# Performance work log

Hardware: AMD Instinct MI355X
Metric: run time of the kernel (lower is better)

The kernel has to match this reference:

```python
import jax, jax.numpy as jnp
import numpy as np

B, N, C, H = 2, 2048, 1024, 16
D = C // H
NEG = -1e9  # keras Softmax large negative for masked positions


def setup_inputs() -> dict:
    key = jax.random.key(0)
    ks = jax.random.split(key, 10)
    s = lambda fan_in: 1.0 / np.sqrt(fan_in)
    return {
        "x": jax.random.normal(ks[0], (B, N, C), jnp.float32),
        "mask": jnp.ones((B, 1, 1, N), jnp.bool_),
        "Wqkv": jax.random.normal(ks[1], (C, 3 * C), jnp.float32) * s(C),
        "bqkv": jnp.zeros((3 * C,), jnp.float32),
        "Wl": jax.random.normal(ks[2], (H, H), jnp.float32) * s(H),
        "bl": jnp.zeros((H,), jnp.float32),
        "Ww": jax.random.normal(ks[3], (H, H), jnp.float32) * s(H),
        "bw": jnp.zeros((H,), jnp.float32),
        "Wp": jax.random.normal(ks[4], (C, C), jnp.float32) * s(C),
        "bp": jnp.zeros((C,), jnp.float32),
    }


def reference(x, mask, Wqkv, bqkv, Wl, bl, Ww, bw, Wp, bp):
    scale = jnp.asarray(D ** -0.5, x.dtype)
    qkv = x @ Wqkv + bqkv                                  # [B,N,3C]
    qkv = qkv.reshape(B, N, 3, H, D).transpose(2, 0, 3, 1, 4)  # [3,B,H,N,D]
    q, k, v = qkv[0] * scale, qkv[1], qkv[2]
    attn = jnp.einsum("bhnd,bhmd->bhnm", q, k)             # [B,H,N,N]
    # pre-softmax talking-heads: mix head axis
    attn = jnp.einsum("bhnm,hg->bgnm", attn, Wl) + bl[None, :, None, None]
    # keras Softmax with boolean mask: add -1e9 where mask is False
    attn = attn + (1.0 - mask.astype(attn.dtype)) * NEG
    attn = jax.nn.softmax(attn, axis=-1)
    # post-softmax talking-heads
    attn = jnp.einsum("bhnm,hg->bgnm", attn, Ww) + bw[None, :, None, None]
    out = jnp.einsum("bhnm,bhmd->bhnd", attn, v)           # [B,H,N,D]
    out = out.transpose(0, 2, 1, 3).reshape(B, N, C)
    return out @ Wp + bp
```

## Files before the change

kernel.cpp:

```cpp
#include <hip/hip_runtime.h>
#include <hip/hip_bf16.h>


typedef __bf16 bf16_t;
typedef __bf16 bf16x8 __attribute__((ext_vector_type(8)));
typedef float f32x4 __attribute__((ext_vector_type(4)));

#define DEV static __device__ __forceinline__

static constexpr float NEGV = -1e9f;

DEV f32x4 mfma16(bf16x8 a, bf16x8 b, f32x4 c) {
  return __builtin_amdgcn_mfma_f32_16x16x32_bf16(a, b, c, 0, 0, 0);
}

DEV bf16x8 zero8() {
  bf16x8 z;
#pragma unroll
  for (int j = 0; j < 8; ++j) z[j] = (bf16_t)0.0f;
  return z;
}

DEV uint32_t pkbf(float lo, float hi) {
  union { bf16_t f; unsigned short s; } a, b;
  a.f = (bf16_t)lo; b.f = (bf16_t)hi;
  return (uint32_t)a.s | ((uint32_t)b.s << 16);
}

union U84 { uint32_t u[4]; bf16x8 v; };

__global__ __launch_bounds__(256) void mask_prep(const unsigned char* __restrict__ raw,
                                                 unsigned char* __restrict__ canon,
                                                 unsigned char* __restrict__ allflag) {
  __shared__ int c0, c12, f0, f1;
  const int tid = threadIdx.x;
  if (tid == 0) { c0 = 0; c12 = 0; f0 = 1; f1 = 1; }
  __syncthreads();
  int l0 = 0, l12 = 0;
  for (int i = tid; i < 4096; i += 256) {
    unsigned char v = raw[i];
    if (v) {
      int r = i & 3;
      if (r == 0) l0++;
      else if (r < 3) l12++;
    }
  }
  if (l0) atomicAdd(&c0, l0);
  if (l12) atomicAdd(&c12, l12);
  __syncthreads();
  const int mode = (c0 == 0) ? 2 : ((c12 > 0) ? 0 : 1);
  for (int i = tid; i < 4096; i += 256) {
    bool t;
    if (mode == 0)      t = raw[i] != 0;
    else if (mode == 1) t = ((const int*)raw)[i] != 0;
    else                t = ((const float*)raw)[i] != 0.0f;
    canon[i] = t ? 1 : 0;
    if (!t) atomicAnd(i < 2048 ? &f0 : &f1, 0);
  }
  __syncthreads();
  if (tid == 0) { allflag[0] = (unsigned char)f0; allflag[1] = (unsigned char)f1; }
}

__global__ __launch_bounds__(256) void gemm_kernel(
    const float* __restrict__ Af, const bf16_t* __restrict__ Ab,
    const float* __restrict__ Bw, const float* __restrict__ bias,
    float* __restrict__ outf,
    bf16_t* __restrict__ Qs, bf16_t* __restrict__ Ks, bf16_t* __restrict__ Vt,
    int K, int Nn, int epi) {
  __shared__ bf16_t As[64][40];
  __shared__ bf16_t Bs[64][40];
  const int tid = threadIdx.x;
  const int lane = tid & 63, wid = tid >> 6;
  const int bx = blockIdx.x, by = blockIdx.y;
  const int wr = (wid >> 1) * 32, wc = (wid & 1) * 32;
  const int lr = lane & 15, kq = lane >> 4;

  f32x4 acc[2][2];
#pragma unroll
  for (int i = 0; i < 2; ++i)
#pragma unroll
    for (int j = 0; j < 2; ++j) acc[i][j] = (f32x4){0.f, 0.f, 0.f, 0.f};

  for (int kt = 0; kt < K; kt += 32) {
    {
      const int row = tid >> 2, c8 = (tid & 3) * 8;
      if (epi == 0) {
        const float* p = Af + (size_t)(bx * 64 + row) * K + kt + c8;
        float4 v0 = *(const float4*)p;
        float4 v1 = *(const float4*)(p + 4);
        bf16x8 v;
        v[0] = (bf16_t)v0.x; v[1] = (bf16_t)v0.y; v[2] = (bf16_t)v0.z; v[3] = (bf16_t)v0.w;
        v[4] = (bf16_t)v1.x; v[5] = (bf16_t)v1.y; v[6] = (bf16_t)v1.z; v[7] = (bf16_t)v1.w;
        *(bf16x8*)&As[row][c8] = v;
      } else {
        *(bf16x8*)&As[row][c8] =
            *(const bf16x8*)(Ab + (size_t)(bx * 64 + row) * K + kt + c8);
      }
      const int krow = tid >> 3, n8 = (tid & 7) * 8;
      const float* bp = Bw + (size_t)(kt + krow) * Nn + by * 64 + n8;
      float4 b0 = *(const float4*)bp;
      float4 b1 = *(const float4*)(bp + 4);
      Bs[n8 + 0][krow] = (bf16_t)b0.x; Bs[n8 + 1][krow] = (bf16_t)b0.y;
      Bs[n8 + 2][krow] = (bf16_t)b0.z; Bs[n8 + 3][krow] = (bf16_t)b0.w;
      Bs[n8 + 4][krow] = (bf16_t)b1.x; Bs[n8 + 5][krow] = (bf16_t)b1.y;
      Bs[n8 + 6][krow] = (bf16_t)b1.z; Bs[n8 + 7][krow] = (bf16_t)b1.w;
    }
    __syncthreads();
#pragma unroll
    for (int rt = 0; rt < 2; ++rt) {
      bf16x8 af = *(const bf16x8*)&As[wr + rt * 16 + lr][kq * 8];
#pragma unroll
      for (int ct = 0; ct < 2; ++ct) {
        bf16x8 bf = *(const bf16x8*)&Bs[wc + ct * 16 + lr][kq * 8];
        acc[rt][ct] = mfma16(af, bf, acc[rt][ct]);
      }
    }
    __syncthreads();
  }

#pragma unroll
  for (int rt = 0; rt < 2; ++rt)
#pragma unroll
    for (int ct = 0; ct < 2; ++ct)
#pragma unroll
      for (int r = 0; r < 4; ++r) {
        const int grow = bx * 64 + wr + rt * 16 + kq * 4 + r;
        const int gcol = by * 64 + wc + ct * 16 + lr;
        const float v = acc[rt][ct][r] + bias[gcol];
        if (epi == 0) {
          const int t = gcol >> 10, h = (gcol >> 6) & 15, d = gcol & 63;
          const int b = grow >> 11, n = grow & 2047;
          if (t == 0)
            Qs[(((size_t)b * 16 + h) * 2048 + n) * 64 + d] = (bf16_t)(v * 0.125f);
          else if (t == 1)
            Ks[(((size_t)b * 16 + h) * 2048 + n) * 64 + d] = (bf16_t)v;
          else
            Vt[(((size_t)b * 16 + h) * 64 + d) * 2048 + n] = (bf16_t)v;
        } else {
          outf[(size_t)grow * Nn + gcol] = v;
        }
      }
}

__global__ __launch_bounds__(256) void vsum_kernel(const bf16_t* __restrict__ Vt,
                                                   float* __restrict__ Vsum) {
  const int lane = threadIdx.x & 63, wid = threadIdx.x >> 6;
  const int row = blockIdx.x * 4 + wid;
  const bf16_t* p = Vt + (size_t)row * 2048;
  float s = 0.f;
#pragma unroll
  for (int it = 0; it < 4; ++it) {
    bf16x8 v = *(const bf16x8*)(p + it * 512 + lane * 8);
#pragma unroll
    for (int j = 0; j < 8; ++j) s += (float)v[j];
  }
#pragma unroll
  for (int off = 32; off; off >>= 1) s += __shfl_xor(s, off);
  if (lane == 0) Vsum[row] = s;
}

__global__ __launch_bounds__(256, 2) void attn_pass1(
    const bf16_t* __restrict__ Qs, const bf16_t* __restrict__ Ks,
    const unsigned char* __restrict__ canon, const unsigned char* __restrict__ allflag,
    const float* __restrict__ Wl, const float* __restrict__ bl,
    float* __restrict__ pstats) {
  __shared__ uint32_t Sb[2][5120];
  const int tid = threadIdx.x, lane = tid & 63, wid = tid >> 6;
  const int c = lane & 15, kq = lane >> 4;
  const int job = (blockIdx.x & 7) * 128 + (blockIdx.x >> 3);
  const int mc = job >> 8, b = (job >> 7) & 1, nt = job & 127;
  const int n0 = nt * 16, mbeg = mc * 512;
  const int h0 = 4 * wid;
  const bool allt = allflag[b] != 0;

  bf16x8 wlf;
#pragma unroll
  for (int j = 0; j < 8; ++j) {
    const int k = kq * 8 + j;
    wlf[j] = (k < 16) ? (bf16_t)Wl[k * 16 + c] : (bf16_t)0.0f;
  }
  f32x4 blv;
#pragma unroll
  for (int r = 0; r < 4; ++r) blv[r] = bl[kq * 4 + r];

  bf16x8 qf[4][2];
#pragma unroll
  for (int hh = 0; hh < 4; ++hh)
#pragma unroll
    for (int ks = 0; ks < 2; ++ks)
      qf[hh][ks] = *(const bf16x8*)(Qs + ((size_t)(b * 16 + h0 + hh) * 2048 + n0 + c) *
                                             64 + ks * 32 + kq * 8);

  auto stage = [&](int v, uint32_t* sb) {
    const int m0 = mbeg + v * 32;
#pragma unroll
    for (int hp = 0; hp < 2; ++hp) {
      bf16x8 kf[2][2][2];
#pragma unroll
      for (int h2 = 0; h2 < 2; ++h2)
#pragma unroll
        for (int mt = 0; mt < 2; ++mt)
#pragma unroll
          for (int ks = 0; ks < 2; ++ks)
            kf[h2][mt][ks] =
                *(const bf16x8*)(Ks + ((size_t)(b * 16 + h0 + hp * 2 + h2) * 2048 +
                                       m0 + mt * 16 + c) * 64 + ks * 32 + kq * 8);
#pragma unroll
      for (int mt = 0; mt < 2; ++mt) {
        f32x4 a0 = (f32x4){0.f, 0.f, 0.f, 0.f};
        f32x4 a1 = (f32x4){0.f, 0.f, 0.f, 0.f};
        a0 = mfma16(qf[hp * 2 + 0][0], kf[0][mt][0], a0);
        a0 = mfma16(qf[hp * 2 + 0][1], kf[0][mt][1], a0);
        a1 = mfma16(qf[hp * 2 + 1][0], kf[1][mt][0], a1);
        a1 = mfma16(qf[hp * 2 + 1][1], kf[1][mt][1], a1);
#pragma unroll
        for (int r = 0; r < 4; ++r) {
          const int p = (kq * 4 + r) * 32 + mt * 16 + c;
          sb[p * 10 + ((2 * wid + hp) ^ (kq & 1))] = pkbf(a0[r], a1[r]);
        }
      }
    }
  };

  auto gatherS = [&](const uint32_t* sb, int pp) {
    const int prow = (wid * 8 + pp) * 16 + c;
    const int bp = (prow >> 7) & 1;
    if (kq < 2) {
      U84 t;
#pragma unroll
      for (int i = 0; i < 4; ++i) t.u[i] = sb[prow * 10 + ((kq * 4 + i) ^ bp)];
      return t.v;
    }
    return zero8();
  };

  float lacc[4][4];
#pragma unroll
  for (int r = 0; r < 4; ++r)
#pragma unroll
    for (int ns = 0; ns < 4; ++ns) lacc[r][ns] = 0.f;

  stage(0, Sb[0]);
  __syncthreads();
  for (int u = 0; u < 16; ++u) {
#pragma unroll
    for (int pp = 0; pp < 8; ++pp) {
      bf16x8 sf = gatherS(Sb[u & 1], pp);
      f32x4 d1 = mfma16(wlf, sf, blv);
      if (!allt && !canon[b * 2048 + mbeg + u * 32 + (pp & 1) * 16 + c]) {
        d1[0] += NEGV; d1[1] += NEGV; d1[2] += NEGV; d1[3] += NEGV;
      }
      const int ns = pp >> 1;
#pragma unroll
      for (int r = 0; r < 4; ++r) lacc[r][ns] += __expf(d1[r]);
    }
    if (u < 15) stage(u + 1, Sb[(u + 1) & 1]);
    __syncthreads();
  }

#pragma unroll
  for (int r = 0; r < 4; ++r)
#pragma unroll
    for (int ns = 0; ns < 4; ++ns) {
      float s = lacc[r][ns];
      s += __shfl_xor(s, 1);
      s += __shfl_xor(s, 2);
      s += __shfl_xor(s, 4);
      s += __shfl_xor(s, 8);
      if (c == 0)
        pstats[((size_t)(b * 4 + mc) * 2048 + n0 + wid * 4 + ns) * 16 + kq * 4 + r] = s;
    }
}

__global__ __launch_bounds__(256) void stats_merge(const float* __restrict__ ps,
                                                   float* __restrict__ fin) {
  const int i = blockIdx.x * 256 + threadIdx.x;
  const int b = i >> 15, rest = i & 32767;
  float s = 0.f;
#pragma unroll
  for (int ch = 0; ch < 4; ++ch) s += ps[((size_t)(b * 4 + ch) << 15) + rest];
  fin[i] = 1.0f / s;
}

__global__ __launch_bounds__(256, 2) void attn_pass2(
    const bf16_t* __restrict__ Qs, const bf16_t* __restrict__ Ks,
    const bf16_t* __restrict__ Vt, const unsigned char* __restrict__ canon,
    const unsigned char* __restrict__ allflag,
    const float* __restrict__ Wl, const float* __restrict__ bl,
    const float* __restrict__ Ww, const float* __restrict__ fin,
    float* __restrict__ Opart) {
  __shared__ uint32_t Sb[2][5120];
  __shared__ uint32_t Fb[2][16 * 260];
  const int tid = threadIdx.x, lane = tid & 63, wid = tid >> 6;
  const int c = lane & 15, kq = lane >> 4;
  const int job = (blockIdx.x & 7) * 64 + (blockIdx.x >> 3);
  const int mc = job >> 8, b = (job >> 7) & 1, nt = job & 127;
  const int n0 = nt * 16, mbeg = mc * 1024;
  const int h0 = 4 * wid;
  const bool allt = allflag[b] != 0;

  bf16x8 wlf, wwf;
#pragma unroll
  for (int j = 0; j < 8; ++j) {
    const int k = kq * 8 + j;
    wlf[j] = (k < 16) ? (bf16_t)Wl[k * 16 + c] : (bf16_t)0.0f;
    wwf[j] = (k < 16) ? (bf16_t)Ww[k * 16 + c] : (bf16_t)0.0f;
  }
  f32x4 blv;
#pragma unroll
  for (int r = 0; r < 4; ++r) blv[r] = bl[kq * 4 + r];

  float4 ivv[4];
#pragma unroll
  for (int ns = 0; ns < 4; ++ns)
    ivv[ns] =
        *(const float4*)&fin[((size_t)b * 2048 + n0 + wid * 4 + ns) * 16 + kq * 4];

  bf16x8 qf[4][2];
#pragma unroll
  for (int hh = 0; hh < 4; ++hh)
#pragma unroll
    for (int ks = 0; ks < 2; ++ks)
      qf[hh][ks] = *(const bf16x8*)(Qs + ((size_t)(b * 16 + h0 + hh) * 2048 + n0 + c) *
                                             64 + ks * 32 + kq * 8);

  auto stage = [&](int v, uint32_t* sb) {
    const int m0 = mbeg + v * 32;
#pragma unroll
    for (int hp = 0; hp < 2; ++hp) {
      bf16x8 kf[2][2][2];
#pragma unroll
      for (int h2 = 0; h2 < 2; ++h2)
#pragma unroll
        for (int mt = 0; mt < 2; ++mt)
#pragma unroll
          for (int ks = 0; ks < 2; ++ks)
            kf[h2][mt][ks] =
                *(const bf16x8*)(Ks + ((size_t)(b * 16 + h0 + hp * 2 + h2) * 2048 +
                                       m0 + mt * 16 + c) * 64 + ks * 32 + kq * 8);
#pragma unroll
      for (int mt = 0; mt < 2; ++mt) {
        f32x4 a0 = (f32x4){0.f, 0.f, 0.f, 0.f};
        f32x4 a1 = (f32x4){0.f, 0.f, 0.f, 0.f};
        a0 = mfma16(qf[hp * 2 + 0][0], kf[0][mt][0], a0);
        a0 = mfma16(qf[hp * 2 + 0][1], kf[0][mt][1], a0);
        a1 = mfma16(qf[hp * 2 + 1][0], kf[1][mt][0], a1);
        a1 = mfma16(qf[hp * 2 + 1][1], kf[1][mt][1], a1);
#pragma unroll
        for (int r = 0; r < 4; ++r) {
          const int p = (kq * 4 + r) * 32 + mt * 16 + c;
          sb[p * 10 + ((2 * wid + hp) ^ (kq & 1))] = pkbf(a0[r], a1[r]);
        }
      }
    }
  };

  auto gatherS = [&](const uint32_t* sb, int pp) {
    const int prow = (wid * 8 + pp) * 16 + c;
    const int bp = (prow >> 7) & 1;
    if (kq < 2) {
      U84 t;
#pragma unroll
      for (int i = 0; i < 4; ++i) t.u[i] = sb[prow * 10 + ((kq * 4 + i) ^ bp)];
      return t.v;
    }
    return zero8();
  };

  f32x4 oacc[4][4];
#pragma unroll
  for (int i = 0; i < 4; ++i)
#pragma unroll
    for (int j = 0; j < 4; ++j) oacc[i][j] = (f32x4){0.f, 0.f, 0.f, 0.f};

  stage(0, Sb[0]);
  __syncthreads();
  for (int u = 0; u < 32; ++u) {
    const uint32_t* scur = Sb[u & 1];
    uint32_t* snxt = Sb[(u + 1) & 1];
    bf16_t* fcur = (bf16_t*)Fb[u & 1];
    const uint32_t* fprev = Fb[(u + 1) & 1];
    if (u > 0) {
#pragma unroll
      for (int hh = 0; hh < 4; ++hh) {
        const int g2 = h0 + hh;
        bf16x8 af = *(const bf16x8*)&fprev[g2 * 260 + c * 16 + ((kq ^ (c & 3)) << 2)];
#pragma unroll
        for (int dt = 0; dt < 4; ++dt) {
          bf16x8 vf = *(const bf16x8*)(Vt + ((size_t)(b * 16 + g2) * 64 + dt * 16 + c) *
                                                2048 + mbeg + (u - 1) * 32 + kq * 8);
          oacc[hh][dt] = mfma16(af, vf, oacc[hh][dt]);
        }
      }
    }
#pragma unroll
    for (int pp = 0; pp < 8; ++pp) {
      bf16x8 sf = gatherS(scur, pp);
      f32x4 d1 = mfma16(wlf, sf, blv);
      if (!allt && !canon[b * 2048 + mbeg + u * 32 + (pp & 1) * 16 + c]) {
        d1[0] += NEGV; d1[1] += NEGV; d1[2] += NEGV; d1[3] += NEGV;
      }
      const int ns = pp >> 1;
      const float e0 = __expf(d1[0]) * ivv[ns].x;
      const float e1 = __expf(d1[1]) * ivv[ns].y;
      const float e2 = __expf(d1[2]) * ivv[ns].z;
      const float e3 = __expf(d1[3]) * ivv[ns].w;
      const uint32_t Aw = pkbf(e0, e1);
      const uint32_t Bw2 = pkbf(e2, e3);
      const int s0 = (c + 32 * kq) & 63;
      const int s1 = (s0 + 16) & 63;
      U84 ef;
      ef.u[0] = (uint32_t)__shfl((int)Aw, s0);
      ef.u[1] = (uint32_t)__shfl((int)Bw2, s0);
      ef.u[2] = (uint32_t)__shfl((int)Aw, s1);
      ef.u[3] = (uint32_t)__shfl((int)Bw2, s1);
      bf16x8 efv = (kq < 2) ? ef.v : zero8();
      f32x4 d2 = mfma16(wwf, efv, (f32x4){0.f, 0.f, 0.f, 0.f});
      const int pg = wid * 8 + pp;
      const int nl = pg >> 1, ml = (pg & 1) * 16 + c;
      const int wm = (ml >> 1) ^ ((nl & 3) << 2);
#pragma unroll
      for (int r = 0; r < 4; ++r)
        fcur[(kq * 4 + r) * 520 + nl * 32 + wm * 2 + (ml & 1)] = (bf16_t)d2[r];
    }
    if (u < 31) stage(u + 1, snxt);
    __syncthreads();
  }
  {
    const uint32_t* fprev = Fb[1];
#pragma unroll
    for (int hh = 0; hh < 4; ++hh) {
      const int g2 = h0 + hh;
      bf16x8 af = *(const bf16x8*)&fprev[g2 * 260 + c * 16 + ((kq ^ (c & 3)) << 2)];
#pragma unroll
      for (int dt = 0; dt < 4; ++dt) {
        bf16x8 vf = *(const bf16x8*)(Vt + ((size_t)(b * 16 + g2) * 64 + dt * 16 + c) *
                                              2048 + mbeg + 31 * 32 + kq * 8);
        oacc[hh][dt] = mfma16(af, vf, oacc[hh][dt]);
      }
    }
  }

#pragma unroll
  for (int hh = 0; hh < 4; ++hh)
#pragma unroll
    for (int dt = 0; dt < 4; ++dt)
#pragma unroll
      for (int r = 0; r < 4; ++r) {
        const int n = n0 + kq * 4 + r;
        const int col = (h0 + hh) * 64 + dt * 16 + c;
        Opart[(((size_t)b * 2 + mc) * 2048 + n) * 1024 + col] = oacc[hh][dt][r];
      }
}

__global__ __launch_bounds__(256) void reduce_ao(const float* __restrict__ Opart,
                                                 const float* __restrict__ bw,
                                                 const float* __restrict__ Vsum,
                                                 bf16_t* __restrict__ AO) {
  const size_t i = ((size_t)blockIdx.x * 256 + threadIdx.x) * 4;
  const int c = (int)(i & 1023), n = (int)((i >> 10) & 2047), b = (int)(i >> 21);
  const float4 p0 = *(const float4*)&Opart[(((size_t)b * 2 + 0) * 2048 + n) * 1024 + c];
  const float4 p1 = *(const float4*)&Opart[(((size_t)b * 2 + 1) * 2048 + n) * 1024 + c];
  float vv[4] = {p0.x + p1.x, p0.y + p1.y, p0.z + p1.z, p0.w + p1.w};
#pragma unroll
  for (int j = 0; j < 4; ++j) {
    const int cj = c + j, g2 = cj >> 6, d = cj & 63;
    AO[i + j] = (bf16_t)(vv[j] + bw[g2] * Vsum[((size_t)b * 16 + g2) * 64 + d]);
  }
}

extern "C" void kernel_launch(void* const* d_in, const int* in_sizes, int n_in,
                              void* d_out, int out_size, void* d_ws, size_t ws_size,
                              hipStream_t stream) {
  const float* x = (const float*)d_in[0];
  const unsigned char* mask = (const unsigned char*)d_in[1];
  const float* Wqkv = (const float*)d_in[2];
  const float* bqkv = (const float*)d_in[3];
  const float* Wl = (const float*)d_in[4];
  const float* bl = (const float*)d_in[5];
  const float* Ww = (const float*)d_in[6];
  const float* bw = (const float*)d_in[7];
  const float* Wp = (const float*)d_in[8];
  const float* bp = (const float*)d_in[9];
  float* out = (float*)d_out;

  char* w = (char*)d_ws;
  auto alloc = [&](size_t bytes) {
    char* p = w;
    w += (bytes + 255) & ~(size_t)255;
    return p;
  };
  bf16_t* Qs = (bf16_t*)alloc((size_t)2 * 16 * 2048 * 64 * 2);
  bf16_t* Ks = (bf16_t*)alloc((size_t)2 * 16 * 2048 * 64 * 2);
  bf16_t* Vt = (bf16_t*)alloc((size_t)2 * 16 * 2048 * 64 * 2);
  bf16_t* AO = (bf16_t*)alloc((size_t)4096 * 1024 * 2);
  float* Opart = (float*)alloc((size_t)4 * 2048 * 1024 * 4);
  float* pstats = (float*)alloc((size_t)8 * 2048 * 16 * 4);
  float* fstats = (float*)alloc((size_t)2 * 2048 * 16 * 4);
  float* Vsum = (float*)alloc((size_t)2048 * 4);
  unsigned char* canon = (unsigned char*)alloc(4096);
  unsigned char* allflag = (unsigned char*)alloc(256);

  mask_prep<<<dim3(1), dim3(256), 0, stream>>>(mask, canon, allflag);
  gemm_kernel<<<dim3(64, 48), dim3(256), 0, stream>>>(
      x, (const bf16_t*)nullptr, Wqkv, bqkv, nullptr, Qs, Ks, Vt, 1024, 3072, 0);
  vsum_kernel<<<dim3(512), dim3(256), 0, stream>>>(Vt, Vsum);
  attn_pass1<<<dim3(1024), dim3(256), 0, stream>>>(Qs, Ks, canon, allflag, Wl, bl,
                                                   pstats);
  stats_merge<<<dim3(256), dim3(256), 0, stream>>>(pstats, fstats);
  attn_pass2<<<dim3(512), dim3(256), 0, stream>>>(Qs, Ks, Vt, canon, allflag, Wl, bl,
                                                  Ww, fstats, Opart);
  reduce_ao<<<dim3(4096), dim3(256), 0, stream>>>(Opart, bw, Vsum, AO);
  gemm_kernel<<<dim3(64, 16), dim3(256), 0, stream>>>(
      (const float*)nullptr, AO, Wp, bp, out, nullptr, nullptr, nullptr, 1024, 1024, 1);
}
```

Baseline: 581.8 us.

## Single-buffer LDS in attention passes to allow four blocks per CU

Both attention kernels drop their double-buffered LDS staging of scores and probabilities. Each now stages the current tile, synchronises, then consumes it, and the PV product runs in the same iteration after an extra barrier. Launch bounds are raised from 2 to 4 blocks per CU, which the halved LDS footprint permits. The aim is more resident waves to hide latency, at the cost of losing the overlap between staging the next tile and computing the current one. It also adds barriers and tighter register limits that may cause spills.

New measurement: 884.6 us. 52.0% more time.

```diff
diff --git a/kernel.cpp b/kernel.cpp
--- a/kernel.cpp
+++ b/kernel.cpp
@@ -159,12 +159,12 @@
   if (lane == 0) Vsum[row] = s;
 }
 
-__global__ __launch_bounds__(256, 2) void attn_pass1(
+__global__ __launch_bounds__(256, 4) void attn_pass1(
     const bf16_t* __restrict__ Qs, const bf16_t* __restrict__ Ks,
     const unsigned char* __restrict__ canon, const unsigned char* __restrict__ allflag,
     const float* __restrict__ Wl, const float* __restrict__ bl,
     float* __restrict__ pstats) {
-  __shared__ uint32_t Sb[2][5120];
+  __shared__ uint32_t Sb[5120];
   const int tid = threadIdx.x, lane = tid & 63, wid = tid >> 6;
   const int c = lane & 15, kq = lane >> 4;
   const int job = (blockIdx.x & 7) * 128 + (blockIdx.x >> 3);
@@ -191,7 +191,7 @@
       qf[hh][ks] = *(const bf16x8*)(Qs + ((size_t)(b * 16 + h0 + hh) * 2048 + n0 + c) *
                                              64 + ks * 32 + kq * 8);
 
-  auto stage = [&](int v, uint32_t* sb) {
+  auto stage = [&](int v) {
     const int m0 = mbeg + v * 32;
 #pragma unroll
     for (int hp = 0; hp < 2; ++hp) {
@@ -216,19 +216,19 @@
 #pragma unroll
         for (int r = 0; r < 4; ++r) {
           const int p = (kq * 4 + r) * 32 + mt * 16 + c;
-          sb[p * 10 + ((2 * wid + hp) ^ (kq & 1))] = pkbf(a0[r], a1[r]);
+          Sb[p * 10 + ((2 * wid + hp) ^ (kq & 1))] = pkbf(a0[r], a1[r]);
         }
       }
     }
   };
 
-  auto gatherS = [&](const uint32_t* sb, int pp) {
+  auto gatherS = [&](int pp) {
     const int prow = (wid * 8 + pp) * 16 + c;
     const int bp = (prow >> 7) & 1;
     if (kq < 2) {
       U84 t;
 #pragma unroll
-      for (int i = 0; i < 4; ++i) t.u[i] = sb[prow * 10 + ((kq * 4 + i) ^ bp)];
+      for (int i = 0; i < 4; ++i) t.u[i] = Sb[prow * 10 + ((kq * 4 + i) ^ bp)];
       return t.v;
     }
     return zero8();
@@ -240,12 +240,12 @@
 #pragma unroll
     for (int ns = 0; ns < 4; ++ns) lacc[r][ns] = 0.f;
 
-  stage(0, Sb[0]);
-  __syncthreads();
   for (int u = 0; u < 16; ++u) {
+    stage(u);
+    __syncthreads();
 #pragma unroll
     for (int pp = 0; pp < 8; ++pp) {
-      bf16x8 sf = gatherS(Sb[u & 1], pp);
+      bf16x8 sf = gatherS(pp);
       f32x4 d1 = mfma16(wlf, sf, blv);
       if (!allt && !canon[b * 2048 + mbeg + u * 32 + (pp & 1) * 16 + c]) {
         d1[0] += NEGV; d1[1] += NEGV; d1[2] += NEGV; d1[3] += NEGV;
@@ -254,7 +254,6 @@
 #pragma unroll
       for (int r = 0; r < 4; ++r) lacc[r][ns] += __expf(d1[r]);
     }
-    if (u < 15) stage(u + 1, Sb[(u + 1) & 1]);
     __syncthreads();
   }
 
@@ -282,15 +281,15 @@
   fin[i] = 1.0f / s;
 }
 
-__global__ __launch_bounds__(256, 2) void attn_pass2(
+__global__ __launch_bounds__(256, 4) void attn_pass2(
     const bf16_t* __restrict__ Qs, const bf16_t* __restrict__ Ks,
     const bf16_t* __restrict__ Vt, const unsigned char* __restrict__ canon,
     const unsigned char* __restrict__ allflag,
     const float* __restrict__ Wl, const float* __restrict__ bl,
     const float* __restrict__ Ww, const float* __restrict__ fin,
     float* __restrict__ Opart) {
-  __shared__ uint32_t Sb[2][5120];
-  __shared__ uint32_t Fb[2][16 * 260];
+  __shared__ uint32_t Sb[5120];
+  __shared__ uint32_t Fb[16 * 260];
   const int tid = threadIdx.x, lane = tid & 63, wid = tid >> 6;
   const int c = lane & 15, kq = lane >> 4;
   const int job = (blockIdx.x & 7) * 64 + (blockIdx.x >> 3);
@@ -324,7 +323,7 @@
       qf[hh][ks] = *(const bf16x8*)(Qs + ((size_t)(b * 16 + h0 + hh) * 2048 + n0 + c) *
                                              64 + ks * 32 + kq * 8);
 
-  auto stage = [&](int v, uint32_t* sb) {
+  auto stage = [&](int v) {
     const int m0 = mbeg + v * 32;
 #pragma unroll
     for (int hp = 0; hp < 2; ++hp) {
@@ -349,19 +348,19 @@
 #pragma unroll
         for (int r = 0; r < 4; ++r) {
           const int p = (kq * 4 + r) * 32 + mt * 16 + c;
-          sb[p * 10 + ((2 * wid + hp) ^ (kq & 1))] = pkbf(a0[r], a1[r]);
+          Sb[p * 10 + ((2 * wid + hp) ^ (kq & 1))] = pkbf(a0[r], a1[r]);
         }
       }
     }
   };
 
-  auto gatherS = [&](const uint32_t* sb, int pp) {
+  auto gatherS = [&](int pp) {
     const int prow = (wid * 8 + pp) * 16 + c;
     const int bp = (prow >> 7) & 1;
     if (kq < 2) {
       U84 t;
 #pragma unroll
-      for (int i = 0; i < 4; ++i) t.u[i] = sb[prow * 10 + ((kq * 4 + i) ^ bp)];
+      for (int i = 0; i < 4; ++i) t.u[i] = Sb[prow * 10 + ((kq * 4 + i) ^ bp)];
       return t.v;
     }
     return zero8();
@@ -373,29 +372,13 @@
 #pragma unroll
     for (int j = 0; j < 4; ++j) oacc[i][j] = (f32x4){0.f, 0.f, 0.f, 0.f};
 
-  stage(0, Sb[0]);
-  __syncthreads();
   for (int u = 0; u < 32; ++u) {
-    const uint32_t* scur = Sb[u & 1];
-    uint32_t* snxt = Sb[(u + 1) & 1];
-    bf16_t* fcur = (bf16_t*)Fb[u & 1];
-    const uint32_t* fprev = Fb[(u + 1) & 1];
-    if (u > 0) {
-#pragma unroll
-      for (int hh = 0; hh < 4; ++hh) {
-        const int g2 = h0 + hh;
-        bf16x8 af = *(const bf16x8*)&fprev[g2 * 260 + c * 16 + ((kq ^ (c & 3)) << 2)];
-#pragma unroll
-        for (int dt = 0; dt < 4; ++dt) {
-          bf16x8 vf = *(const bf16x8*)(Vt + ((size_t)(b * 16 + g2) * 64 + dt * 16 + c) *
-                                                2048 + mbeg + (u - 1) * 32 + kq * 8);
-          oacc[hh][dt] = mfma16(af, vf, oacc[hh][dt]);
-        }
-      }
-    }
+    stage(u);
+    __syncthreads();
+    bf16_t* fcur = (bf16_t*)Fb;
 #pragma unroll
     for (int pp = 0; pp < 8; ++pp) {
-      bf16x8 sf = gatherS(scur, pp);
+      bf16x8 sf = gatherS(pp);
       f32x4 d1 = mfma16(wlf, sf, blv);
       if (!allt && !canon[b * 2048 + mbeg + u * 32 + (pp & 1) * 16 + c]) {
         d1[0] += NEGV; d1[1] += NEGV; d1[2] += NEGV; d1[3] += NEGV;
@@ -423,19 +406,15 @@
       for (int r = 0; r < 4; ++r)
         fcur[(kq * 4 + r) * 520 + nl * 32 + wm * 2 + (ml & 1)] = (bf16_t)d2[r];
     }
-    if (u < 31) stage(u + 1, snxt);
-    __syncthreads();
-  }
-  {
-    const uint32_t* fprev = Fb[1];
+    __syncthreads();
 #pragma unroll
     for (int hh = 0; hh < 4; ++hh) {
       const int g2 = h0 + hh;
-      bf16x8 af = *(const bf16x8*)&fprev[g2 * 260 + c * 16 + ((kq ^ (c & 3)) << 2)];
+      bf16x8 af = *(const bf16x8*)&Fb[g2 * 260 + c * 16 + ((kq ^ (c & 3)) << 2)];
 #pragma unroll
       for (int dt = 0; dt < 4; ++dt) {
         bf16x8 vf = *(const bf16x8*)(Vt + ((size_t)(b * 16 + g2) * 64 + dt * 16 + c) *
-                                              2048 + mbeg + 31 * 32 + kq * 8);
+                                              2048 + mbeg + u * 32 + kq * 8);
         oacc[hh][dt] = mfma16(af, vf, oacc[hh][dt]);
       }
     }
```
